# Performance work log

Measured on AMD Instinct MI355X. Metric: run time of the kernel, lower is better.

Reference implementation:

```python
import jax, jax.numpy as jnp
import numpy as np

NEG_INF = -1e9  # mask fill value used by the original module


def setup_inputs() -> dict:
    key = jax.random.key(0)
    k1, k2 = jax.random.split(key)
    max_T, B, S, D = 16, 8, 2048, 1024
    entries = jax.random.normal(k1, (max_T, B, S, D), dtype=jnp.float32)
    proj = jax.random.normal(k2, (max_T, D), dtype=jnp.float32)
    norm_scale = jnp.ones((D,), dtype=jnp.float32)
    return {
        "entries": entries,
        "proj": proj,
        "norm_scale": norm_scale,
        "n_active": 12,
        "block_idx": 12,
    }


def reference(entries, proj, norm_scale, n_active, block_idx):
    """Depth-wise attention over block outputs.

    entries:    [max_T, B, S, d]
    proj:       [max_T, d]  (pseudo-query table)
    norm_scale: [d]
    Returns [B, S, d].
    """
    max_T = entries.shape[0]
    norm_eps = 1e-5
    query = proj[min(block_idx, max_T - 1)]  # [d]
    # Per-entry RMSNorm (keys only; values stay unnormed)
    rms = jnp.sqrt(jnp.mean(entries ** 2, axis=-1, keepdims=True) + norm_eps)
    normed = entries / rms * norm_scale[None, None, None, :]
    # Scores over depth dim
    logits = jnp.einsum('d,tbsd->tbs', query, normed)
    mask = jnp.arange(max_T)[:, None, None] < n_active
    logits = jnp.where(mask, logits, NEG_INF)
    weights = jax.nn.softmax(logits, axis=0)  # [max_T, B, S]
    return jnp.einsum('tbs,tbsd->bsd', weights, entries)
```

## Files before the change

### kernel.cpp

```cpp
#include <hip/hip_runtime.h>

#define MAXT 16
#define DDIM 1024
#define NTHREADS 256
#define TPW 4

__device__ __forceinline__ float dpp_sum64(float x) {
    int v;
    v = __builtin_amdgcn_update_dpp(0, __float_as_int(x), 0x111, 0xf, 0xf, true);
    x += __int_as_float(v);
    v = __builtin_amdgcn_update_dpp(0, __float_as_int(x), 0x112, 0xf, 0xf, true);
    x += __int_as_float(v);
    v = __builtin_amdgcn_update_dpp(0, __float_as_int(x), 0x114, 0xf, 0xf, true);
    x += __int_as_float(v);
    v = __builtin_amdgcn_update_dpp(0, __float_as_int(x), 0x118, 0xf, 0xf, true);
    x += __int_as_float(v);
    v = __builtin_amdgcn_update_dpp(0, __float_as_int(x), 0x142, 0xa, 0xf, false);
    x += __int_as_float(v);
    v = __builtin_amdgcn_update_dpp(0, __float_as_int(x), 0x143, 0xc, 0xf, false);
    x += __int_as_float(v);
    return __int_as_float(__builtin_amdgcn_readlane(__float_as_int(x), 63));
}

__global__ __launch_bounds__(NTHREADS, 3)
void attn_depth_kernel(const float* __restrict__ entries,
                       const float* __restrict__ proj,
                       const float* __restrict__ norm_scale,
                       const int* __restrict__ n_active_p,
                       const int* __restrict__ block_idx_p,
                       float* __restrict__ out,
                       int BS)
{
    const int site = blockIdx.x;
    const int tid  = threadIdx.x;
    const int wave = tid >> 6;
    const int lane = tid & 63;

    int n_act = *n_active_p;
    n_act = n_act < 1 ? 1 : (n_act > MAXT ? MAXT : n_act);
    int row = *block_idx_p;
    row = row > (MAXT - 1) ? (MAXT - 1) : (row < 0 ? 0 : row);

    const int dbase = lane * 4;

    const size_t tStride = (size_t)BS * DDIM;
    const float* ebase = entries + (size_t)site * DDIM + dbase;

    float4 e[TPW][4];
#pragma unroll
    for (int tt = 0; tt < TPW; ++tt) {
        const int t = wave + 4 * tt;
        if (t < n_act) {
#pragma unroll
            for (int c = 0; c < 4; ++c)
                e[tt][c] = *reinterpret_cast<const float4*>(ebase + (size_t)t * tStride + c * 256);
        } else {
#pragma unroll
            for (int c = 0; c < 4; ++c)
                e[tt][c] = make_float4(0.f, 0.f, 0.f, 0.f);
        }
    }

    float4 q[4];
#pragma unroll
    for (int c = 0; c < 4; ++c) {
        float4 p  = *reinterpret_cast<const float4*>(proj + (size_t)row * DDIM + c * 256 + dbase);
        float4 ns = *reinterpret_cast<const float4*>(norm_scale + c * 256 + dbase);
        q[c] = make_float4(p.x * ns.x, p.y * ns.y, p.z * ns.z, p.w * ns.w);
    }

    float ss[TPW], dt[TPW];
#pragma unroll
    for (int tt = 0; tt < TPW; ++tt) {
        float s = 0.f, d = 0.f;
#pragma unroll
        for (int c = 0; c < 4; ++c) {
            const float4 v = e[tt][c];
            s = fmaf(v.x, v.x, s); s = fmaf(v.y, v.y, s);
            s = fmaf(v.z, v.z, s); s = fmaf(v.w, v.w, s);
            d = fmaf(q[c].x, v.x, d); d = fmaf(q[c].y, v.y, d);
            d = fmaf(q[c].z, v.z, d); d = fmaf(q[c].w, v.w, d);
        }
        ss[tt] = s; dt[tt] = d;
    }

#pragma unroll
    for (int tt = 0; tt < TPW; ++tt) {
        ss[tt] = dpp_sum64(ss[tt]);
        dt[tt] = dpp_sum64(dt[tt]);
    }

    __shared__ float red[2 * MAXT];
    __shared__ float part[TPW][DDIM];

    if (lane == 0) {
#pragma unroll
        for (int tt = 0; tt < TPW; ++tt) {
            const int t = wave + 4 * tt;
            red[t]        = ss[tt];
            red[MAXT + t] = dt[tt];
        }
    }
    __syncthreads();

    float lg[MAXT];
    float4 rs[4], rd[4];
#pragma unroll
    for (int c = 0; c < 4; ++c) {
        rs[c] = *reinterpret_cast<const float4*>(&red[c * 4]);
        rd[c] = *reinterpret_cast<const float4*>(&red[MAXT + c * 4]);
    }
#pragma unroll
    for (int c = 0; c < 4; ++c) {
        lg[c * 4 + 0] = rd[c].x * rsqrtf(rs[c].x * (1.f / DDIM) + 1e-5f);
        lg[c * 4 + 1] = rd[c].y * rsqrtf(rs[c].y * (1.f / DDIM) + 1e-5f);
        lg[c * 4 + 2] = rd[c].z * rsqrtf(rs[c].z * (1.f / DDIM) + 1e-5f);
        lg[c * 4 + 3] = rd[c].w * rsqrtf(rs[c].w * (1.f / DDIM) + 1e-5f);
    }
    float m = -3.0e38f;
#pragma unroll
    for (int t = 0; t < MAXT; ++t)
        if (t < n_act) m = fmaxf(m, lg[t]);
    float sum = 0.f;
#pragma unroll
    for (int t = 0; t < MAXT; ++t)
        if (t < n_act) sum += __expf(lg[t] - m);
    const float inv = 1.f / sum;

    float wt[TPW];
#pragma unroll
    for (int tt = 0; tt < TPW; ++tt) {
        const int t = wave + 4 * tt;
        const float s_ = red[t];
        const float d_ = red[MAXT + t];
        const float l_ = d_ * rsqrtf(s_ * (1.f / DDIM) + 1e-5f);
        wt[tt] = (t < n_act) ? __expf(l_ - m) * inv : 0.f;
    }

    float4 acc[4];
#pragma unroll
    for (int c = 0; c < 4; ++c) acc[c] = make_float4(0.f, 0.f, 0.f, 0.f);
#pragma unroll
    for (int tt = 0; tt < TPW; ++tt) {
#pragma unroll
        for (int c = 0; c < 4; ++c) {
            acc[c].x = fmaf(wt[tt], e[tt][c].x, acc[c].x);
            acc[c].y = fmaf(wt[tt], e[tt][c].y, acc[c].y);
            acc[c].z = fmaf(wt[tt], e[tt][c].z, acc[c].z);
            acc[c].w = fmaf(wt[tt], e[tt][c].w, acc[c].w);
        }
    }
#pragma unroll
    for (int c = 0; c < 4; ++c)
        *reinterpret_cast<float4*>(&part[wave][c * 256 + dbase]) = acc[c];
    __syncthreads();

    const int od = tid * 4;
    float4 r0 = *reinterpret_cast<const float4*>(&part[0][od]);
    float4 r1 = *reinterpret_cast<const float4*>(&part[1][od]);
    float4 r2 = *reinterpret_cast<const float4*>(&part[2][od]);
    float4 r3 = *reinterpret_cast<const float4*>(&part[3][od]);
    float4 r;
    r.x = (r0.x + r1.x) + (r2.x + r3.x);
    r.y = (r0.y + r1.y) + (r2.y + r3.y);
    r.z = (r0.z + r1.z) + (r2.z + r3.z);
    r.w = (r0.w + r1.w) + (r2.w + r3.w);
    *reinterpret_cast<float4*>(out + (size_t)site * DDIM + od) = r;
}

extern "C" void kernel_launch(void* const* d_in, const int* in_sizes, int n_in,
                              void* d_out, int out_size, void* d_ws, size_t ws_size,
                              hipStream_t stream)
{
    const float* entries = (const float*)d_in[0];
    const float* proj    = (const float*)d_in[1];
    const float* nscale  = (const float*)d_in[2];
    const int*   n_act   = (const int*)d_in[3];
    const int*   bidx    = (const int*)d_in[4];
    float*       out     = (float*)d_out;

    const int BS = out_size / DDIM;
    attn_depth_kernel<<<BS, NTHREADS, 0, stream>>>(entries, proj, nscale,
                                                   n_act, bidx, out, BS);
}
```

Baseline: 162.4 us.

## Process eight sites per block with double-buffered register prefetch

Each block now handles eight (b,s) sites instead of one. While one site is reduced, the entries for the next site are already being loaded into a second register buffer, so global-load latency can overlap with reduction work. The query projection is computed once per block instead of once per site. Loads for inactive depth slots are clamped to the last active slot rather than branched around, and the block barriers now use an explicit lgkmcnt wait. In exchange, the doubled register footprint forces launch bounds down to 2 blocks per SIMD, lowering occupancy on a kernel that is already near memory bandwidth.

```diff
diff --git a/kernel.cpp b/kernel.cpp
--- a/kernel.cpp
+++ b/kernel.cpp
@@ -4,6 +4,10 @@
 #define DDIM 1024
 #define NTHREADS 256
 #define TPW 4
+#define SPB 8
+
+#define LGKM_BAR() do { asm volatile("s_waitcnt lgkmcnt(0)" ::: "memory"); \
+                        __builtin_amdgcn_s_barrier(); } while (0)
 
 __device__ __forceinline__ float dpp_sum64(float x) {
     int v;
@@ -22,53 +26,26 @@
     return __int_as_float(__builtin_amdgcn_readlane(__float_as_int(x), 63));
 }
 
-__global__ __launch_bounds__(NTHREADS, 3)
-void attn_depth_kernel(const float* __restrict__ entries,
-                       const float* __restrict__ proj,
-                       const float* __restrict__ norm_scale,
-                       const int* __restrict__ n_active_p,
-                       const int* __restrict__ block_idx_p,
-                       float* __restrict__ out,
-                       int BS)
-{
-    const int site = blockIdx.x;
-    const int tid  = threadIdx.x;
-    const int wave = tid >> 6;
-    const int lane = tid & 63;
-
-    int n_act = *n_active_p;
-    n_act = n_act < 1 ? 1 : (n_act > MAXT ? MAXT : n_act);
-    int row = *block_idx_p;
-    row = row > (MAXT - 1) ? (MAXT - 1) : (row < 0 ? 0 : row);
-
-    const int dbase = lane * 4;
-
-    const size_t tStride = (size_t)BS * DDIM;
-    const float* ebase = entries + (size_t)site * DDIM + dbase;
-
-    float4 e[TPW][4];
-#pragma unroll
-    for (int tt = 0; tt < TPW; ++tt) {
-        const int t = wave + 4 * tt;
-        if (t < n_act) {
-#pragma unroll
-            for (int c = 0; c < 4; ++c)
-                e[tt][c] = *reinterpret_cast<const float4*>(ebase + (size_t)t * tStride + c * 256);
-        } else {
-#pragma unroll
-            for (int c = 0; c < 4; ++c)
-                e[tt][c] = make_float4(0.f, 0.f, 0.f, 0.f);
-        }
-    }
-
-    float4 q[4];
-#pragma unroll
-    for (int c = 0; c < 4; ++c) {
-        float4 p  = *reinterpret_cast<const float4*>(proj + (size_t)row * DDIM + c * 256 + dbase);
-        float4 ns = *reinterpret_cast<const float4*>(norm_scale + c * 256 + dbase);
-        q[c] = make_float4(p.x * ns.x, p.y * ns.y, p.z * ns.z, p.w * ns.w);
-    }
-
+__device__ __forceinline__
+void load_site(float4 (&e)[TPW][4], const float* __restrict__ ebase,
+               size_t tStride, int wave, int n1)
+{
+#pragma unroll
+    for (int tt = 0; tt < TPW; ++tt) {
+        const int t  = wave + 4 * tt;
+        const int tl = t <= n1 ? t : n1;
+#pragma unroll
+        for (int c = 0; c < 4; ++c)
+            e[tt][c] = *reinterpret_cast<const float4*>(ebase + (size_t)tl * tStride + c * 256);
+    }
+}
+
+__device__ __forceinline__
+void process_site(const float4 (&e)[TPW][4], const float4 (&q)[4],
+                  float* __restrict__ red, float (* __restrict__ part)[DDIM],
+                  int wave, int lane, int tid, int dbase, int n_act,
+                  float* __restrict__ osite)
+{
     float ss[TPW], dt[TPW];
 #pragma unroll
     for (int tt = 0; tt < TPW; ++tt) {
@@ -90,9 +67,6 @@
         dt[tt] = dpp_sum64(dt[tt]);
     }
 
-    __shared__ float red[2 * MAXT];
-    __shared__ float part[TPW][DDIM];
-
     if (lane == 0) {
 #pragma unroll
         for (int tt = 0; tt < TPW; ++tt) {
@@ -101,21 +75,17 @@
             red[MAXT + t] = dt[tt];
         }
     }
-    __syncthreads();
+    LGKM_BAR();
 
     float lg[MAXT];
-    float4 rs[4], rd[4];
 #pragma unroll
     for (int c = 0; c < 4; ++c) {
-        rs[c] = *reinterpret_cast<const float4*>(&red[c * 4]);
-        rd[c] = *reinterpret_cast<const float4*>(&red[MAXT + c * 4]);
-    }
-#pragma unroll
-    for (int c = 0; c < 4; ++c) {
-        lg[c * 4 + 0] = rd[c].x * rsqrtf(rs[c].x * (1.f / DDIM) + 1e-5f);
-        lg[c * 4 + 1] = rd[c].y * rsqrtf(rs[c].y * (1.f / DDIM) + 1e-5f);
-        lg[c * 4 + 2] = rd[c].z * rsqrtf(rs[c].z * (1.f / DDIM) + 1e-5f);
-        lg[c * 4 + 3] = rd[c].w * rsqrtf(rs[c].w * (1.f / DDIM) + 1e-5f);
+        const float4 rs = *reinterpret_cast<const float4*>(&red[c * 4]);
+        const float4 rd = *reinterpret_cast<const float4*>(&red[MAXT + c * 4]);
+        lg[c * 4 + 0] = rd.x * rsqrtf(rs.x * (1.f / DDIM) + 1e-5f);
+        lg[c * 4 + 1] = rd.y * rsqrtf(rs.y * (1.f / DDIM) + 1e-5f);
+        lg[c * 4 + 2] = rd.z * rsqrtf(rs.z * (1.f / DDIM) + 1e-5f);
+        lg[c * 4 + 3] = rd.w * rsqrtf(rs.w * (1.f / DDIM) + 1e-5f);
     }
     float m = -3.0e38f;
 #pragma unroll
@@ -153,19 +123,75 @@
 #pragma unroll
     for (int c = 0; c < 4; ++c)
         *reinterpret_cast<float4*>(&part[wave][c * 256 + dbase]) = acc[c];
-    __syncthreads();
+    LGKM_BAR();
 
     const int od = tid * 4;
-    float4 r0 = *reinterpret_cast<const float4*>(&part[0][od]);
-    float4 r1 = *reinterpret_cast<const float4*>(&part[1][od]);
-    float4 r2 = *reinterpret_cast<const float4*>(&part[2][od]);
-    float4 r3 = *reinterpret_cast<const float4*>(&part[3][od]);
+    const float4 r0 = *reinterpret_cast<const float4*>(&part[0][od]);
+    const float4 r1 = *reinterpret_cast<const float4*>(&part[1][od]);
+    const float4 r2 = *reinterpret_cast<const float4*>(&part[2][od]);
+    const float4 r3 = *reinterpret_cast<const float4*>(&part[3][od]);
     float4 r;
     r.x = (r0.x + r1.x) + (r2.x + r3.x);
     r.y = (r0.y + r1.y) + (r2.y + r3.y);
     r.z = (r0.z + r1.z) + (r2.z + r3.z);
     r.w = (r0.w + r1.w) + (r2.w + r3.w);
-    *reinterpret_cast<float4*>(out + (size_t)site * DDIM + od) = r;
+    *reinterpret_cast<float4*>(osite + od) = r;
+}
+
+__global__ __launch_bounds__(NTHREADS, 2)
+void attn_depth_kernel(const float* __restrict__ entries,
+                       const float* __restrict__ proj,
+                       const float* __restrict__ norm_scale,
+                       const int* __restrict__ n_active_p,
+                       const int* __restrict__ block_idx_p,
+                       float* __restrict__ out,
+                       int BS)
+{
+    const int tid   = threadIdx.x;
+    const int wave  = tid >> 6;
+    const int lane  = tid & 63;
+    const int dbase = lane * 4;
+
+    int n_act = *n_active_p;
+    n_act = n_act < 1 ? 1 : (n_act > MAXT ? MAXT : n_act);
+    const int n1 = n_act - 1;
+    int row = *block_idx_p;
+    row = row > (MAXT - 1) ? (MAXT - 1) : (row < 0 ? 0 : row);
+
+    float4 q[4];
+#pragma unroll
+    for (int c = 0; c < 4; ++c) {
+        const float4 p  = *reinterpret_cast<const float4*>(proj + (size_t)row * DDIM + c * 256 + dbase);
+        const float4 ns = *reinterpret_cast<const float4*>(norm_scale + c * 256 + dbase);
+        q[c] = make_float4(p.x * ns.x, p.y * ns.y, p.z * ns.z, p.w * ns.w);
+    }
+
+    __shared__ float red[2 * MAXT];
+    __shared__ float part[TPW][DDIM];
+
+    const size_t tStride = (size_t)BS * DDIM;
+    const size_t site0   = (size_t)blockIdx.x * SPB;
+
+    size_t s_[SPB];
+#pragma unroll
+    for (int k = 0; k < SPB; ++k) {
+        size_t s = site0 + (size_t)k;
+        s_[k] = s < (size_t)BS ? s : (size_t)(BS - 1);
+    }
+
+    float4 eA[TPW][4], eB[TPW][4];
+    load_site(eA, entries + s_[0] * DDIM + dbase, tStride, wave, n1);
+
+#pragma unroll
+    for (int p = 0; p < SPB / 2; ++p) {
+        load_site(eB, entries + s_[2 * p + 1] * DDIM + dbase, tStride, wave, n1);
+        process_site(eA, q, red, part, wave, lane, tid, dbase, n_act,
+                     out + s_[2 * p] * DDIM);
+        if (p + 1 < SPB / 2)
+            load_site(eA, entries + s_[2 * p + 2] * DDIM + dbase, tStride, wave, n1);
+        process_site(eB, q, red, part, wave, lane, tid, dbase, n_act,
+                     out + s_[2 * p + 1] * DDIM);
+    }
 }
 
 extern "C" void kernel_launch(void* const* d_in, const int* in_sizes, int n_in,
@@ -179,7 +205,8 @@
     const int*   bidx    = (const int*)d_in[4];
     float*       out     = (float*)d_out;
 
-    const int BS = out_size / DDIM;
-    attn_depth_kernel<<<BS, NTHREADS, 0, stream>>>(entries, proj, nscale,
-                                                   n_act, bidx, out, BS);
-}
+    const int BS   = out_size / DDIM;
+    const int nblk = (BS + SPB - 1) / SPB;
+    attn_depth_kernel<<<nblk, NTHREADS, 0, stream>>>(entries, proj, nscale,
+                                                     n_act, bidx, out, BS);
+}
```

Result: slower. 181.3 us (+11.6%).

## Map one wave per site with online softmax and double-buffered entry loads

Applied to the files above, without the earlier changes.

Each wavefront now handles a whole site and iterates over depth entries, streaming two entries at a time with an online-softmax running max and rescaled accumulator. This removes the shared-memory reductions and both block-wide barriers of the previous layout, which split the depth entries across waves. The cost is fewer outstanding loads per wave (two entries in flight instead of all of them), a serial dependency chain over depth, and extra exp/rescale work per entry.

```diff
diff --git a/kernel.cpp b/kernel.cpp
--- a/kernel.cpp
+++ b/kernel.cpp
@@ -3,7 +3,7 @@
 #define MAXT 16
 #define DDIM 1024
 #define NTHREADS 256
-#define TPW 4
+#define WPB (NTHREADS / 64)
 
 __device__ __forceinline__ float dpp_sum64(float x) {
     int v;
@@ -22,150 +22,132 @@
     return __int_as_float(__builtin_amdgcn_readlane(__float_as_int(x), 63));
 }
 
-__global__ __launch_bounds__(NTHREADS, 3)
-void attn_depth_kernel(const float* __restrict__ entries,
-                       const float* __restrict__ proj,
-                       const float* __restrict__ norm_scale,
-                       const int* __restrict__ n_active_p,
-                       const int* __restrict__ block_idx_p,
-                       float* __restrict__ out,
-                       int BS)
+__global__ __launch_bounds__(NTHREADS, 4)
+void attn_wave_site_kernel(const float* __restrict__ entries,
+                           const float* __restrict__ proj,
+                           const float* __restrict__ norm_scale,
+                           const int* __restrict__ n_active_p,
+                           const int* __restrict__ block_idx_p,
+                           float* __restrict__ out,
+                           int BS)
 {
-    const int site = blockIdx.x;
-    const int tid  = threadIdx.x;
-    const int wave = tid >> 6;
-    const int lane = tid & 63;
+    const int tid   = threadIdx.x;
+    const int wave  = tid >> 6;
+    const int lane  = tid & 63;
+    const int site  = blockIdx.x * WPB + wave;
+    const int dbase = lane * 4;
 
     int n_act = *n_active_p;
     n_act = n_act < 1 ? 1 : (n_act > MAXT ? MAXT : n_act);
     int row = *block_idx_p;
     row = row > (MAXT - 1) ? (MAXT - 1) : (row < 0 ? 0 : row);
 
-    const int dbase = lane * 4;
+    float4 q[4];
+#pragma unroll
+    for (int c = 0; c < 4; ++c) {
+        const float4 p  = *reinterpret_cast<const float4*>(proj + (size_t)row * DDIM + c * 256 + dbase);
+        const float4 ns = *reinterpret_cast<const float4*>(norm_scale + c * 256 + dbase);
+        q[c] = make_float4(p.x * ns.x, p.y * ns.y, p.z * ns.z, p.w * ns.w);
+    }
 
     const size_t tStride = (size_t)BS * DDIM;
-    const float* ebase = entries + (size_t)site * DDIM + dbase;
+    const float* eb = entries + (size_t)site * DDIM + dbase;
 
-    float4 e[TPW][4];
+    float4 A[4], B[4];
 #pragma unroll
-    for (int tt = 0; tt < TPW; ++tt) {
-        const int t = wave + 4 * tt;
-        if (t < n_act) {
+    for (int c = 0; c < 4; ++c)
+        A[c] = *reinterpret_cast<const float4*>(eb + c * 256);
+    if (1 < n_act) {
 #pragma unroll
-            for (int c = 0; c < 4; ++c)
-                e[tt][c] = *reinterpret_cast<const float4*>(ebase + (size_t)t * tStride + c * 256);
-        } else {
+        for (int c = 0; c < 4; ++c)
+            B[c] = *reinterpret_cast<const float4*>(eb + tStride + c * 256);
+    }
+
+    float  m    = -3.0e38f;
+    float  ssum = 0.f;
+    float4 acc[4];
 #pragma unroll
-            for (int c = 0; c < 4; ++c)
-                e[tt][c] = make_float4(0.f, 0.f, 0.f, 0.f);
+    for (int c = 0; c < 4; ++c) acc[c] = make_float4(0.f, 0.f, 0.f, 0.f);
+
+#pragma unroll
+    for (int tp = 0; tp < MAXT / 2; ++tp) {
+        const int t0 = 2 * tp;
+        const int t1 = 2 * tp + 1;
+
+        if (t0 < n_act) {
+            float s = 0.f, d = 0.f;
+#pragma unroll
+            for (int c = 0; c < 4; ++c) {
+                s = fmaf(A[c].x, A[c].x, s); s = fmaf(A[c].y, A[c].y, s);
+                s = fmaf(A[c].z, A[c].z, s); s = fmaf(A[c].w, A[c].w, s);
+                d = fmaf(q[c].x, A[c].x, d); d = fmaf(q[c].y, A[c].y, d);
+                d = fmaf(q[c].z, A[c].z, d); d = fmaf(q[c].w, A[c].w, d);
+            }
+            s = dpp_sum64(s);
+            d = dpp_sum64(d);
+            const float l  = d * rsqrtf(s * (1.f / DDIM) + 1e-5f);
+            const float mn = fmaxf(m, l);
+            const float cs = __expf(m - mn);
+            const float w  = __expf(l - mn);
+            ssum = fmaf(ssum, cs, w);
+            m = mn;
+#pragma unroll
+            for (int c = 0; c < 4; ++c) {
+                acc[c].x = fmaf(acc[c].x, cs, w * A[c].x);
+                acc[c].y = fmaf(acc[c].y, cs, w * A[c].y);
+                acc[c].z = fmaf(acc[c].z, cs, w * A[c].z);
+                acc[c].w = fmaf(acc[c].w, cs, w * A[c].w);
+            }
+            if (t0 + 2 < n_act) {
+#pragma unroll
+                for (int c = 0; c < 4; ++c)
+                    A[c] = *reinterpret_cast<const float4*>(eb + (size_t)(t0 + 2) * tStride + c * 256);
+            }
+        }
+
+        if (t1 < n_act) {
+            float s = 0.f, d = 0.f;
+#pragma unroll
+            for (int c = 0; c < 4; ++c) {
+                s = fmaf(B[c].x, B[c].x, s); s = fmaf(B[c].y, B[c].y, s);
+                s = fmaf(B[c].z, B[c].z, s); s = fmaf(B[c].w, B[c].w, s);
+                d = fmaf(q[c].x, B[c].x, d); d = fmaf(q[c].y, B[c].y, d);
+                d = fmaf(q[c].z, B[c].z, d); d = fmaf(q[c].w, B[c].w, d);
+            }
+            s = dpp_sum64(s);
+            d = dpp_sum64(d);
+            const float l  = d * rsqrtf(s * (1.f / DDIM) + 1e-5f);
+            const float mn = fmaxf(m, l);
+            const float cs = __expf(m - mn);
+            const float w  = __expf(l - mn);
+            ssum = fmaf(ssum, cs, w);
+            m = mn;
+#pragma unroll
+            for (int c = 0; c < 4; ++c) {
+                acc[c].x = fmaf(acc[c].x, cs, w * B[c].x);
+                acc[c].y = fmaf(acc[c].y, cs, w * B[c].y);
+                acc[c].z = fmaf(acc[c].z, cs, w * B[c].z);
+                acc[c].w = fmaf(acc[c].w, cs, w * B[c].w);
+            }
+            if (t1 + 2 < n_act) {
+#pragma unroll
+                for (int c = 0; c < 4; ++c)
+                    B[c] = *reinterpret_cast<const float4*>(eb + (size_t)(t1 + 2) * tStride + c * 256);
+            }
         }
     }
 
-    float4 q[4];
+    const float inv = 1.f / ssum;
+    float* ob = out + (size_t)site * DDIM + dbase;
 #pragma unroll
     for (int c = 0; c < 4; ++c) {
-        float4 p  = *reinterpret_cast<const float4*>(proj + (size_t)row * DDIM + c * 256 + dbase);
-        float4 ns = *reinterpret_cast<const float4*>(norm_scale + c * 256 + dbase);
-        q[c] = make_float4(p.x * ns.x, p.y * ns.y, p.z * ns.z, p.w * ns.w);
+        float4 r;
+        r.x = acc[c].x * inv;
+        r.y = acc[c].y * inv;
+        r.z = acc[c].z * inv;
+        r.w = acc[c].w * inv;
+        *reinterpret_cast<float4*>(ob + c * 256) = r;
     }
-
-    float ss[TPW], dt[TPW];
-#pragma unroll
-    for (int tt = 0; tt < TPW; ++tt) {
-        float s = 0.f, d = 0.f;
-#pragma unroll
-        for (int c = 0; c < 4; ++c) {
-            const float4 v = e[tt][c];
-            s = fmaf(v.x, v.x, s); s = fmaf(v.y, v.y, s);
-            s = fmaf(v.z, v.z, s); s = fmaf(v.w, v.w, s);
-            d = fmaf(q[c].x, v.x, d); d = fmaf(q[c].y, v.y, d);
-            d = fmaf(q[c].z, v.z, d); d = fmaf(q[c].w, v.w, d);
-        }
-        ss[tt] = s; dt[tt] = d;
-    }
-
-#pragma unroll
-    for (int tt = 0; tt < TPW; ++tt) {
-        ss[tt] = dpp_sum64(ss[tt]);
-        dt[tt] = dpp_sum64(dt[tt]);
-    }
-
-    __shared__ float red[2 * MAXT];
-    __shared__ float part[TPW][DDIM];
-
-    if (lane == 0) {
-#pragma unroll
-        for (int tt = 0; tt < TPW; ++tt) {
-            const int t = wave + 4 * tt;
-            red[t]        = ss[tt];
-            red[MAXT + t] = dt[tt];
-        }
-    }
-    __syncthreads();
-
-    float lg[MAXT];
-    float4 rs[4], rd[4];
-#pragma unroll
-    for (int c = 0; c < 4; ++c) {
-        rs[c] = *reinterpret_cast<const float4*>(&red[c * 4]);
-        rd[c] = *reinterpret_cast<const float4*>(&red[MAXT + c * 4]);
-    }
-#pragma unroll
-    for (int c = 0; c < 4; ++c) {
-        lg[c * 4 + 0] = rd[c].x * rsqrtf(rs[c].x * (1.f / DDIM) + 1e-5f);
-        lg[c * 4 + 1] = rd[c].y * rsqrtf(rs[c].y * (1.f / DDIM) + 1e-5f);
-        lg[c * 4 + 2] = rd[c].z * rsqrtf(rs[c].z * (1.f / DDIM) + 1e-5f);
-        lg[c * 4 + 3] = rd[c].w * rsqrtf(rs[c].w * (1.f / DDIM) + 1e-5f);
-    }
-    float m = -3.0e38f;
-#pragma unroll
-    for (int t = 0; t < MAXT; ++t)
-        if (t < n_act) m = fmaxf(m, lg[t]);
-    float sum = 0.f;
-#pragma unroll
-    for (int t = 0; t < MAXT; ++t)
-        if (t < n_act) sum += __expf(lg[t] - m);
-    const float inv = 1.f / sum;
-
-    float wt[TPW];
-#pragma unroll
-    for (int tt = 0; tt < TPW; ++tt) {
-        const int t = wave + 4 * tt;
-        const float s_ = red[t];
-        const float d_ = red[MAXT + t];
-        const float l_ = d_ * rsqrtf(s_ * (1.f / DDIM) + 1e-5f);
-        wt[tt] = (t < n_act) ? __expf(l_ - m) * inv : 0.f;
-    }
-
-    float4 acc[4];
-#pragma unroll
-    for (int c = 0; c < 4; ++c) acc[c] = make_float4(0.f, 0.f, 0.f, 0.f);
-#pragma unroll
-    for (int tt = 0; tt < TPW; ++tt) {
-#pragma unroll
-        for (int c = 0; c < 4; ++c) {
-            acc[c].x = fmaf(wt[tt], e[tt][c].x, acc[c].x);
-            acc[c].y = fmaf(wt[tt], e[tt][c].y, acc[c].y);
-            acc[c].z = fmaf(wt[tt], e[tt][c].z, acc[c].z);
-            acc[c].w = fmaf(wt[tt], e[tt][c].w, acc[c].w);
-        }
-    }
-#pragma unroll
-    for (int c = 0; c < 4; ++c)
-        *reinterpret_cast<float4*>(&part[wave][c * 256 + dbase]) = acc[c];
-    __syncthreads();
-
-    const int od = tid * 4;
-    float4 r0 = *reinterpret_cast<const float4*>(&part[0][od]);
-    float4 r1 = *reinterpret_cast<const float4*>(&part[1][od]);
-    float4 r2 = *reinterpret_cast<const float4*>(&part[2][od]);
-    float4 r3 = *reinterpret_cast<const float4*>(&part[3][od]);
-    float4 r;
-    r.x = (r0.x + r1.x) + (r2.x + r3.x);
-    r.y = (r0.y + r1.y) + (r2.y + r3.y);
-    r.z = (r0.z + r1.z) + (r2.z + r3.z);
-    r.w = (r0.w + r1.w) + (r2.w + r3.w);
-    *reinterpret_cast<float4*>(out + (size_t)site * DDIM + od) = r;
 }
 
 extern "C" void kernel_launch(void* const* d_in, const int* in_sizes, int n_in,
@@ -180,6 +162,6 @@
     float*       out     = (float*)d_out;
 
     const int BS = out_size / DDIM;
-    attn_depth_kernel<<<BS, NTHREADS, 0, stream>>>(entries, proj, nscale,
-                                                   n_act, bidx, out, BS);
+    attn_wave_site_kernel<<<BS / WPB, NTHREADS, 0, stream>>>(entries, proj, nscale,
+                                                             n_act, bidx, out, BS);
 }
```

New measurement: 165.0 us. Within noise of the previous version (+1.6%).
